# Optimization experiments

Hardware: AMD Instinct MI355X
Metric: run time of the kernel (lower is better)

The kernel has to match this reference:

```python
import jax, jax.numpy as jnp
import numpy as np
import math

B, S, D, H = 2, 2048, 1024, 16
DH = D // H          # 64 head dim
BLK = 64             # SpargeAttn block size
TOPK = 0.5           # fraction of KV blocks kept per query block
NEG = -1e9


def setup_inputs() -> dict:
    key = jax.random.key(0)
    ks = jax.random.split(key, 8)
    s = 0.02
    return {
        "inputs": jax.random.normal(ks[0], (B, S, D), dtype=jnp.float32),
        "ln_g": jnp.ones((D,), jnp.float32),
        "ln_b": jnp.zeros((D,), jnp.float32),
        "Wq": jax.random.normal(ks[1], (D, D), jnp.float32) * s,
        "bq": jnp.zeros((D,), jnp.float32),
        "Wk": jax.random.normal(ks[2], (D, D), jnp.float32) * s,
        "bk": jnp.zeros((D,), jnp.float32),
        "Wv": jax.random.normal(ks[3], (D, D), jnp.float32) * s,
        "bv": jnp.zeros((D,), jnp.float32),
        "Wo": jax.random.normal(ks[4], (D, D), jnp.float32) * s,
        "bo": jnp.zeros((D,), jnp.float32),
    }


def _sparse_topk_attn(q, k, v):
    # q,k,v: [B,H,S,DH]. Block-mean-similarity top-k sparse causal attention
    # (SpargeAttn spas_sage2_attn_meansim_topk, fp32 reference semantics).
    nb = S // BLK
    qm = q.reshape(B, H, nb, BLK, DH).mean(3)          # [B,H,nb,DH]
    km = k.reshape(B, H, nb, BLK, DH).mean(3)
    sim = jnp.einsum('bhqd,bhkd->bhqk', qm, km)        # block similarity
    cblk = jnp.tril(jnp.ones((nb, nb), bool))          # causal block mask
    sim = jnp.where(cblk, sim, NEG)
    kk = max(1, int(math.ceil(TOPK * nb)))
    _, idx = jax.lax.top_k(sim, kk)                    # [B,H,nb,kk]
    blk = jax.nn.one_hot(idx, nb, dtype=jnp.float32).sum(-2) > 0  # [B,H,nb,nb]
    blk = (blk & cblk) | jnp.eye(nb, dtype=bool)       # keep diagonal block
    tok_mask = jnp.repeat(jnp.repeat(blk, BLK, axis=2), BLK, axis=3)  # [B,H,S,S]
    tok_mask = tok_mask & jnp.tril(jnp.ones((S, S), bool))
    scores = jnp.einsum('bhid,bhjd->bhij', q, k) / jnp.float32(math.sqrt(DH))
    scores = jnp.where(tok_mask, scores, NEG)
    p = jax.nn.softmax(scores, axis=-1)
    return jnp.einsum('bhij,bhjd->bhid', p, v)


def reference(inputs, ln_g, ln_b, Wq, bq, Wk, bk, Wv, bv, Wo, bo):
    # pre-norm LayerNorm
    mu = inputs.mean(-1, keepdims=True)
    var = inputs.var(-1, keepdims=True)
    x = (inputs - mu) * jax.lax.rsqrt(var + 1e-5) * ln_g + ln_b
    # QKV projections -> [B,H,S,DH]
    q = (x @ Wq + bq).reshape(B, S, H, DH).transpose(0, 2, 1, 3)
    k = (x @ Wk + bk).reshape(B, S, H, DH).transpose(0, 2, 1, 3)
    v = (x @ Wv + bv).reshape(B, S, H, DH).transpose(0, 2, 1, 3)
    ctx = _sparse_topk_attn(q, k, v)
    ctx = ctx.transpose(0, 2, 1, 3).reshape(B, S, D)
    return ctx @ Wo + bo
```

## Files before the change

kernel.cpp:

```cpp
#include <hip/hip_runtime.h>
#include <stdint.h>

#define DEV static __device__ __forceinline__

typedef __attribute__((ext_vector_type(8))) short s16x8;
typedef __attribute__((ext_vector_type(4))) float f32x4;

constexpr int Bdim = 2, Sdim = 2048, Ddim = 1024, Hdim = 16, DH = 64;
constexpr int Mrows = Bdim * Sdim;
constexpr int NB = 32;
constexpr int SEL_STRIDE = 18;

constexpr size_t OFF_XB    = 0;
constexpr size_t OFF_WTQKV = OFF_XB    + (size_t)Mrows*Ddim*2;
constexpr size_t OFF_WOT   = OFF_WTQKV + (size_t)3072*1024*2;
constexpr size_t OFF_QKV   = OFF_WOT   + (size_t)1024*1024*2;
constexpr size_t OFF_CTX   = OFF_QKV   + (size_t)Mrows*3072*2;
constexpr size_t OFF_XM    = OFF_CTX   + (size_t)Mrows*Ddim*2;
constexpr size_t OFF_QM    = OFF_XM    + (size_t)64*1024*4;
constexpr size_t OFF_KM    = OFF_QM    + (size_t)64*1024*4;
constexpr size_t OFF_BIASQ = OFF_KM    + (size_t)64*1024*4;
constexpr size_t OFF_SEL   = OFF_BIASQ + (size_t)3072*4;
constexpr size_t OFF_PART  = OFF_SEL   + (size_t)1024*SEL_STRIDE*4;

DEV float bf2f(unsigned short u){ union{unsigned int i; float f;} x; x.i = ((unsigned int)u)<<16; return x.f; }
DEV unsigned short f2bf(float f){ union{float f; unsigned int i;} x; x.f=f;
  unsigned int r = x.i + 0x7fffu + ((x.i>>16)&1u); return (unsigned short)(r>>16); }

DEV void gload16(const unsigned short* g, unsigned short* l){
  __builtin_amdgcn_global_load_lds(
      (__attribute__((address_space(1))) void*)(void*)g,
      (__attribute__((address_space(3))) void*)l, 16, 0, 0);
}

DEV unsigned int cvtpk(float a, float b){
  unsigned int r;
  asm("v_cvt_pk_bf16_f32 %0, %1, %2" : "=v"(r) : "v"(a), "v"(b));
  return r;
}

__global__ __launch_bounds__(256) void ln_kernel(const float* __restrict__ inp,
                                                 const float* __restrict__ gam,
                                                 const float* __restrict__ bet,
                                                 unsigned short* __restrict__ xb){
  const int row = blockIdx.x, t = threadIdx.x;
  __shared__ float red[8];
  const float4 v = ((const float4*)(inp + (size_t)row*Ddim))[t];
  float s  = v.x + v.y + v.z + v.w;
  float s2 = v.x*v.x + v.y*v.y + v.z*v.z + v.w*v.w;
#pragma unroll
  for (int mk=32; mk>=1; mk>>=1){ s += __shfl_xor(s, mk); s2 += __shfl_xor(s2, mk); }
  if ((t&63)==0){ red[t>>6] = s; red[4+(t>>6)] = s2; }
  __syncthreads();
  s  = red[0]+red[1]+red[2]+red[3];
  s2 = red[4]+red[5]+red[6]+red[7];
  const float mu  = s * (1.f/Ddim);
  const float var = s2 * (1.f/Ddim) - mu*mu;
  const float rs  = rsqrtf(var + 1e-5f);
  const float4 gv = ((const float4*)gam)[t];
  const float4 bv = ((const float4*)bet)[t];
  float o0 = (v.x-mu)*rs*gv.x + bv.x;
  float o1 = (v.y-mu)*rs*gv.y + bv.y;
  float o2 = (v.z-mu)*rs*gv.z + bv.z;
  float o3 = (v.w-mu)*rs*gv.w + bv.w;
  uint2 u;
  u.x = (unsigned int)f2bf(o0) | ((unsigned int)f2bf(o1)<<16);
  u.y = (unsigned int)f2bf(o2) | ((unsigned int)f2bf(o3)<<16);
  ((uint2*)(xb + (size_t)row*Ddim))[t] = u;
}

__global__ __launch_bounds__(256) void xm_kernel(const float* __restrict__ inp,
                                                 const float* __restrict__ gam,
                                                 const float* __restrict__ bet,
                                                 float* __restrict__ xm){
  const int blk = blockIdx.x, t = threadIdx.x;
  const int w = t>>6, lane = t&63;
  __shared__ float part[4][1024];
  float4 gv[4], bv[4];
#pragma unroll
  for (int p=0;p<4;++p){ gv[p] = ((const float4*)gam)[lane + 64*p];
                         bv[p] = ((const float4*)bet)[lane + 64*p]; }
  float ax[4][4];
#pragma unroll
  for (int p=0;p<4;++p)
#pragma unroll
    for (int c=0;c<4;++c) ax[p][c]=0.f;
  for (int rr=0; rr<16; ++rr){
    const int row = blk*64 + w*16 + rr;
    const float4* rp = (const float4*)(inp + (size_t)row*Ddim);
    float4 v[4]; float s=0.f, s2=0.f;
#pragma unroll
    for (int p=0;p<4;++p){
      v[p] = rp[lane + 64*p];
      s  += v[p].x+v[p].y+v[p].z+v[p].w;
      s2 += v[p].x*v[p].x+v[p].y*v[p].y+v[p].z*v[p].z+v[p].w*v[p].w;
    }
#pragma unroll
    for (int mk=32; mk>=1; mk>>=1){ s += __shfl_xor(s,mk); s2 += __shfl_xor(s2,mk); }
    const float mu = s*(1.f/Ddim);
    const float var = s2*(1.f/Ddim) - mu*mu;
    const float rs = rsqrtf(var + 1e-5f);
#pragma unroll
    for (int p=0;p<4;++p){
      ax[p][0] += (v[p].x-mu)*rs*gv[p].x + bv[p].x;
      ax[p][1] += (v[p].y-mu)*rs*gv[p].y + bv[p].y;
      ax[p][2] += (v[p].z-mu)*rs*gv[p].z + bv[p].z;
      ax[p][3] += (v[p].w-mu)*rs*gv[p].w + bv[p].w;
    }
  }
#pragma unroll
  for (int p=0;p<4;++p){
    float4 o; o.x=ax[p][0]; o.y=ax[p][1]; o.z=ax[p][2]; o.w=ax[p][3];
    ((float4*)&part[w][0])[lane + 64*p] = o;
  }
  __syncthreads();
  float4 r0 = ((float4*)&part[0][0])[t];
  float4 r1 = ((float4*)&part[1][0])[t];
  float4 r2 = ((float4*)&part[2][0])[t];
  float4 r3 = ((float4*)&part[3][0])[t];
  float4 o;
  o.x = (r0.x+r1.x+r2.x+r3.x)*(1.f/64);
  o.y = (r0.y+r1.y+r2.y+r3.y)*(1.f/64);
  o.z = (r0.z+r1.z+r2.z+r3.z)*(1.f/64);
  o.w = (r0.w+r1.w+r2.w+r3.w)*(1.f/64);
  ((float4*)(xm + (size_t)blk*Ddim))[t] = o;
}

__global__ __launch_bounds__(256) void wtrans4_kernel(const float* __restrict__ Wq,
                                                      const float* __restrict__ Wk,
                                                      const float* __restrict__ Wv,
                                                      const float* __restrict__ Wo,
                                                      const float* __restrict__ bq,
                                                      const float* __restrict__ bk,
                                                      const float* __restrict__ bv,
                                                      unsigned short* __restrict__ wtqkv,
                                                      unsigned short* __restrict__ wot,
                                                      float* __restrict__ bqkv){
  __shared__ float tile[32][33];
  const int z = blockIdx.z;
  const float* W = (z==0)?Wq:(z==1)?Wk:(z==2)?Wv:Wo;
  unsigned short* Wt = (z<3) ? (wtqkv + (size_t)z*1024*1024) : wot;
  const int n0 = blockIdx.x*32, k0 = blockIdx.y*32;
  const int t = threadIdx.x, r = t>>5, c = t&31;
  if (z<3 && blockIdx.x==0 && blockIdx.y==0){
    const float* bb = (z==0)?bq:(z==1)?bk:bv;
#pragma unroll
    for (int i=0;i<4;++i) bqkv[z*1024 + t + 256*i] = bb[t + 256*i];
  }
#pragma unroll
  for (int i=0;i<4;++i) tile[r+8*i][c] = W[(size_t)(k0 + r + 8*i)*1024 + n0 + c];
  __syncthreads();
#pragma unroll
  for (int i=0;i<4;++i) Wt[(size_t)(n0 + r + 8*i)*1024 + k0 + c] = f2bf(tile[c][r+8*i]);
}

__global__ __launch_bounds__(256) void qmkm_part(const float* __restrict__ xm,
    const float* __restrict__ Wq, const float* __restrict__ Wk,
    float* __restrict__ part){
  const int c  = blockIdx.x*256 + threadIdx.x;
  const int rg = blockIdx.y >> 3, ks = blockIdx.y & 7;
  const int z  = blockIdx.z;
  const float* W = z ? Wk : Wq;
  const int r0 = rg*16, k0 = ks*128;
  float acc[16];
#pragma unroll
  for (int r=0;r<16;++r) acc[r]=0.f;
  for (int k=0;k<128;k+=4){
    const float wv0 = W[(size_t)(k0+k  )*1024 + c];
    const float wv1 = W[(size_t)(k0+k+1)*1024 + c];
    const float wv2 = W[(size_t)(k0+k+2)*1024 + c];
    const float wv3 = W[(size_t)(k0+k+3)*1024 + c];
#pragma unroll
    for (int r=0;r<16;++r){
      const float4 xv = *(const float4*)&xm[(size_t)(r0+r)*1024 + k0 + k];
      acc[r] = fmaf(xv.w, wv3, fmaf(xv.z, wv2, fmaf(xv.y, wv1, fmaf(xv.x, wv0, acc[r]))));
    }
  }
  float* dst = part + (((size_t)z*8 + ks)*64 + r0)*1024 + c;
#pragma unroll
  for (int r=0;r<16;++r) dst[(size_t)r*1024] = acc[r];
}

__global__ __launch_bounds__(256) void qmkm_reduce(const float* __restrict__ part,
    const float* __restrict__ bq, const float* __restrict__ bk,
    float* __restrict__ qm, float* __restrict__ km){
  const int idx = blockIdx.x*256 + threadIdx.x;
  const int z = blockIdx.y;
  const int c = idx & 1023, r = idx >> 10;
  const float* p = part + ((size_t)z*8*64*1024) + (size_t)r*1024 + c;
  float s = 0.f;
#pragma unroll
  for (int ks=0; ks<8; ++ks) s += p[(size_t)ks*64*1024];
  s += z ? bk[c] : bq[c];
  (z ? km : qm)[(size_t)r*1024 + c] = s;
}

__global__ __launch_bounds__(256) void topk_kernel(const float* __restrict__ qm,
                                                   const float* __restrict__ km,
                                                   int* __restrict__ sel){
  const int bhq = blockIdx.x;
  const int qb = bhq & 31, h = (bhq>>5) & 15, b = bhq >> 9;
  const int t = threadIdx.x;
  __shared__ float sim[32];
  __shared__ int keep[32];
  const int kb = t>>3, l8 = t&7;
  float acc = 0.f;
  if (kb <= qb){
    const float* qv = qm + (size_t)(b*32 + qb)*1024 + h*64;
    const float* kv = km + (size_t)(b*32 + kb)*1024 + h*64;
#pragma unroll
    for (int d=0; d<8; ++d) acc += qv[l8*8+d] * kv[l8*8+d];
  }
  acc += __shfl_xor(acc,1); acc += __shfl_xor(acc,2); acc += __shfl_xor(acc,4);
  if (l8==0) sim[kb] = (kb<=qb) ? acc : -1e30f;
  __syncthreads();
  if (t < 32){
    int k2 = t; int ok = 0;
    if (k2 <= qb){
      float sv = sim[k2]; int rank = 0;
      for (int j=0;j<=qb;++j){
        float sj = sim[j];
        rank += (sj > sv) || (sj == sv && j < k2);
      }
      ok = (rank < 16) || (k2 == qb);
    }
    keep[t] = ok;
  }
  __syncthreads();
  if (t == 0){
    int* dstp = sel + (size_t)bhq * SEL_STRIDE;
    int c = 0;
    for (int j=0;j<32;++j) if (keep[j]) dstp[1+c++] = j;
    dstp[0] = c;
  }
}

#define G_STAGE(bsel, kofs) do { \
  gload16(A0 + (kofs), ldsA + (bsel)*4096 + (wid*2+0)*512); \
  gload16(A1 + (kofs), ldsA + (bsel)*4096 + (wid*2+1)*512); \
  gload16(B0 + (kofs), ldsB + (bsel)*4096 + (wid*2+0)*512); \
  gload16(B1 + (kofs), ldsB + (bsel)*4096 + (wid*2+1)*512); \
} while(0)

#define G_COMPUTE(bsel) do { \
  s16x8 af[4], bfr[4]; \
  _Pragma("unroll") \
  for (int mi=0;mi<4;++mi){ \
    int row = wr*64 + mi*16 + rl; \
    af[mi] = *(const s16x8*)((char*)ldsA + (bsel)*8192 + row*64 + ((g ^ ((row>>1)&3))<<4)); \
  } \
  _Pragma("unroll") \
  for (int ni=0;ni<4;++ni){ \
    int row = wc*64 + ni*16 + rl; \
    bfr[ni] = *(const s16x8*)((char*)ldsB + (bsel)*8192 + row*64 + ((g ^ ((row>>1)&3))<<4)); \
  } \
  _Pragma("unroll") \
  for (int mi=0;mi<4;++mi) \
    _Pragma("unroll") \
    for (int ni=0;ni<4;++ni) \
      acc[mi][ni] = __builtin_amdgcn_mfma_f32_16x16x32_bf16(af[mi], bfr[ni], acc[mi][ni], 0,0,0); \
} while(0)

template<int OUT_BF16>
__global__ __launch_bounds__(256) void gemm_bt(const unsigned short* __restrict__ A,
                                               const unsigned short* __restrict__ Bt,
                                               const float* __restrict__ bias,
                                               void* __restrict__ C, int N){
  constexpr int K = 1024;
  __shared__ unsigned short ldsA[2*128*32];
  __shared__ unsigned short ldsB[2*128*32];
  const int t = threadIdx.x, lane = t & 63, wid = t >> 6;
  const int wr = wid >> 1, wc = wid & 1;
  const int rl = lane & 15, g = lane >> 4;

  const int nbx = gridDim.x;
  const int nwg = nbx * gridDim.y;
  const int id  = blockIdx.y * nbx + blockIdx.x;
  const int nid = (id & 7) * (nwg >> 3) + (id >> 3);
  const int m0 = (nid / nbx) * 128, n0 = (nid % nbx) * 128;

  const f32x4 ZERO4 = {0.f,0.f,0.f,0.f};
  f32x4 acc[4][4];
#pragma unroll
  for (int i=0;i<4;++i)
#pragma unroll
    for (int j=0;j<4;++j) acc[i][j] = ZERO4;

  const int slot0 = wid*128 + lane, slot1 = slot0 + 64;
  const int sr0 = slot0>>2, sc0 = slot0&3;
  const int sr1 = slot1>>2, sc1 = slot1&3;
  const unsigned short* A0 = A  + (size_t)(m0 + sr0)*K + (sc0 ^ ((sr0>>1)&3))*8;
  const unsigned short* A1 = A  + (size_t)(m0 + sr1)*K + (sc1 ^ ((sr1>>1)&3))*8;
  const unsigned short* B0 = Bt + (size_t)(n0 + sr0)*K + (sc0 ^ ((sr0>>1)&3))*8;
  const unsigned short* B1 = Bt + (size_t)(n0 + sr1)*K + (sc1 ^ ((sr1>>1)&3))*8;

  G_STAGE(0, 0);
  __syncthreads();

  for (int k0=0; k0<K; k0+=64){
    G_STAGE(1, k0+32);
    G_COMPUTE(0);
    __syncthreads();
    if (k0+64 < K) G_STAGE(0, k0+64);
    G_COMPUTE(1);
    __syncthreads();
  }

  const int r4 = g*4;
#pragma unroll
  for (int mi=0;mi<4;++mi){
#pragma unroll
    for (int ni=0;ni<4;++ni){
      int col = n0 + wc*64 + ni*16 + rl;
      float bb = bias[col];
#pragma unroll
      for (int e=0;e<4;++e){
        int row = m0 + wr*64 + mi*16 + r4 + e;
        float v = acc[mi][ni][e] + bb;
        if (OUT_BF16) ((unsigned short*)C)[(size_t)row*N + col] = f2bf(v);
        else          ((float*)C)[(size_t)row*N + col] = v;
      }
    }
  }
}

__global__ __launch_bounds__(256) void attn_kernel(const unsigned short* __restrict__ qkv,
                                                   const int* __restrict__ sel,
                                                   unsigned short* __restrict__ ctx){
  const int id = blockIdx.x;
  const int xcd = id & 7, jj = id >> 3;
  const int bh = xcd + 8*(jj/24);
  const int tau = jj % 24;
  const int h = bh & 15, b = bh >> 4;
  int qbl[2]; int nq;
  if (tau < 8){ qbl[0]=tau; qbl[1]=15-tau; nq=2; }
  else        { qbl[0]=tau+8; qbl[1]=0;    nq=1; }

  const int t = threadIdx.x, wid = t >> 6, lane = t & 63;
  const int rl = lane & 15, g = lane >> 4;
  const int q_local = wid*16 + rl;

  __shared__ unsigned short K_s[2][4096];
  __shared__ unsigned short V_s[2][4096];

  const int jst = t >> 2, cq = t & 3;
  const int r2 = t >> 3, dq = t & 7;
  const unsigned short* kbase = qkv + (size_t)(b*Sdim + jst)*3072 + 1024 + h*DH + cq*16;
  const unsigned short* vbase = qkv + (size_t)(b*Sdim + 2*r2)*3072 + 2048 + h*DH + dq*8;
  const int kwb0 = jst*128 + (((cq*2  ) ^ (jst&7))<<4);
  const int kwb1 = jst*128 + (((cq*2+1) ^ (jst&7))<<4);
  const f32x4 ZERO4 = {0.f,0.f,0.f,0.f};

  const int src0 = (rl + 16*((2*g  ) & 3)) << 2;
  const int src1 = (rl + 16*((2*g+1) & 3)) << 2;
  const bool hsel = (g >> 1);

  for (int iq=0; iq<nq; ++iq){
    const int qb = qbl[iq];
    const int* selrow = sel + (size_t)(((b*Hdim)+h)*NB + qb) * SEL_STRIDE;
    const int ns = selrow[0];

    const int qg0 = b*Sdim + qb*64 + q_local;
    const unsigned short* qbase = qkv + (size_t)qg0*3072 + h*DH;
    s16x8 qa[2];
#pragma unroll
    for (int kk=0; kk<2; ++kk){
      s16x8 raw = *(const s16x8*)(qbase + kk*32 + g*8);
      s16x8 qq;
#pragma unroll
      for (int e=0;e<8;++e) qq[e] = (short)f2bf(bf2f((unsigned short)raw[e]) * 0.125f);
      qa[kk] = qq;
    }

    f32x4 o[4];
    float m_r = -3.0e38f, l_r = 0.f;
#pragma unroll
    for (int f=0; f<4; ++f) o[f] = ZERO4;

    __syncthreads();

    int kb = selrow[1];
    s16x8 kr0, kr1, vr0, vr1;
    {
      const size_t off = (size_t)kb*64*3072;
      kr0 = *(const s16x8*)(kbase + off);
      kr1 = *(const s16x8*)(kbase + off + 8);
      vr0 = *(const s16x8*)(vbase + off);
      vr1 = *(const s16x8*)(vbase + off + 3072);
    }

    for (int it=0; it<ns; ++it){
      const int buf = it & 1;
      unsigned short* Kw = &K_s[buf][0];
      unsigned short* Vw = &V_s[buf][0];
      *(s16x8*)((char*)Kw + kwb0) = kr0;
      *(s16x8*)((char*)Kw + kwb1) = kr1;
#pragma unroll
      for (int e=0;e<8;++e){
        const int d1 = dq*8 + e;
        const int sw = (d1&7) ^ (d1>>3);
        const unsigned int pr = (unsigned int)(unsigned short)vr0[e]
                              | ((unsigned int)(unsigned short)vr1[e] << 16);
        *(unsigned int*)((char*)Vw + d1*128 + ((4*r2) ^ (sw<<4))) = pr;
      }
      const int kbcur = kb;
      if (it+1 < ns){
        kb = selrow[2+it];
        const size_t off = (size_t)kb*64*3072;
        kr0 = *(const s16x8*)(kbase + off);
        kr1 = *(const s16x8*)(kbase + off + 8);
        vr0 = *(const s16x8*)(vbase + off);
        vr1 = *(const s16x8*)(vbase + off + 3072);
      }
      __syncthreads();

      f32x4 sfT[4];
#pragma unroll
      for (int f=0;f<4;++f) sfT[f] = ZERO4;
#pragma unroll
      for (int kk=0;kk<2;++kk){
#pragma unroll
        for (int f=0;f<4;++f){
          const int jr = f*16 + rl;
          s16x8 kf = *(const s16x8*)((char*)Kw + jr*128 + (((kk*4+g) ^ (jr&7))<<4));
          sfT[f] = __builtin_amdgcn_mfma_f32_16x16x32_bf16(kf, qa[kk], sfT[f], 0,0,0);
        }
      }
      if (kbcur == qb){
#pragma unroll
        for (int f=0;f<4;++f)
#pragma unroll
          for (int e=0;e<4;++e){
            const int j = f*16 + g*4 + e;
            if (j > q_local) sfT[f][e] = -1e9f;
          }
      }
      {
        float mx = sfT[0][0];
#pragma unroll
        for (int f=0;f<4;++f)
#pragma unroll
          for (int e=0;e<4;++e) mx = fmaxf(mx, sfT[f][e]);
        mx = fmaxf(mx, __shfl_xor(mx, 16));
        mx = fmaxf(mx, __shfl_xor(mx, 32));
        const float mn = fmaxf(m_r, mx);
        const float al = __expf(m_r - mn);
        m_r = mn;
        float rs = 0.f;
#pragma unroll
        for (int f=0;f<4;++f)
#pragma unroll
          for (int e=0;e<4;++e){
            const float p = __expf(sfT[f][e] - mn);
            sfT[f][e] = p; rs += p;
          }
        rs += __shfl_xor(rs, 16);
        rs += __shfl_xor(rs, 32);
        l_r = l_r*al + rs;
#pragma unroll
        for (int f=0;f<4;++f)
#pragma unroll
          for (int e=0;e<4;++e) o[f][e] *= al;
      }

      unsigned int plo[4], phi[4];
#pragma unroll
      for (int f=0;f<4;++f){
        plo[f] = cvtpk(sfT[f][0], sfT[f][1]);
        phi[f] = cvtpk(sfT[f][2], sfT[f][3]);
      }

#pragma unroll
      for (int kk=0;kk<2;++kk){
        const int f0 = 2*kk, f1 = 2*kk+1;
        unsigned int a0, b0, w0, w1, w2, w3;
        a0 = __builtin_amdgcn_ds_bpermute(src0, plo[f0]);
        b0 = __builtin_amdgcn_ds_bpermute(src0, plo[f1]);
        w0 = hsel ? b0 : a0;
        a0 = __builtin_amdgcn_ds_bpermute(src0, phi[f0]);
        b0 = __builtin_amdgcn_ds_bpermute(src0, phi[f1]);
        w1 = hsel ? b0 : a0;
        a0 = __builtin_amdgcn_ds_bpermute(src1, plo[f0]);
        b0 = __builtin_amdgcn_ds_bpermute(src1, plo[f1]);
        w2 = hsel ? b0 : a0;
        a0 = __builtin_amdgcn_ds_bpermute(src1, phi[f0]);
        b0 = __builtin_amdgcn_ds_bpermute(src1, phi[f1]);
        w3 = hsel ? b0 : a0;
        union { unsigned int u[4]; s16x8 v; } pfc;
        pfc.u[0] = w0; pfc.u[1] = w1; pfc.u[2] = w2; pfc.u[3] = w3;
        const s16x8 pf = pfc.v;
#pragma unroll
        for (int f=0;f<4;++f){
          const int d = f*16 + rl;
          const int sw = (d&7) ^ (d>>3);
          s16x8 vf = *(const s16x8*)((char*)Vw + d*128 + ((64*kk + 16*g) ^ (sw<<4)));
          o[f] = __builtin_amdgcn_mfma_f32_16x16x32_bf16(vf, pf, o[f], 0,0,0);
        }
      }
    }

    {
      const float inv = 1.f / l_r;
      unsigned short* crow = ctx + (size_t)qg0*Ddim + h*DH;
#pragma unroll
      for (int f=0;f<4;++f){
        uint2 st;
        st.x = (unsigned int)f2bf(o[f][0]*inv) | ((unsigned int)f2bf(o[f][1]*inv)<<16);
        st.y = (unsigned int)f2bf(o[f][2]*inv) | ((unsigned int)f2bf(o[f][3]*inv)<<16);
        *(uint2*)(crow + f*16 + g*4) = st;
      }
    }
  }
}

extern "C" void kernel_launch(void* const* d_in, const int* in_sizes, int n_in,
                              void* d_out, int out_size, void* d_ws, size_t ws_size,
                              hipStream_t stream){
  (void)in_sizes; (void)n_in; (void)out_size; (void)ws_size;
  const float* inp  = (const float*)d_in[0];
  const float* ln_g = (const float*)d_in[1];
  const float* ln_b = (const float*)d_in[2];
  const float* Wq   = (const float*)d_in[3];
  const float* bq   = (const float*)d_in[4];
  const float* Wk   = (const float*)d_in[5];
  const float* bk   = (const float*)d_in[6];
  const float* Wv   = (const float*)d_in[7];
  const float* bv   = (const float*)d_in[8];
  const float* Wo   = (const float*)d_in[9];
  const float* bo   = (const float*)d_in[10];

  char* ws = (char*)d_ws;
  unsigned short* xb    = (unsigned short*)(ws + OFF_XB);
  unsigned short* wtqkv = (unsigned short*)(ws + OFF_WTQKV);
  unsigned short* wot   = (unsigned short*)(ws + OFF_WOT);
  unsigned short* qkvb  = (unsigned short*)(ws + OFF_QKV);
  unsigned short* ctx   = (unsigned short*)(ws + OFF_CTX);
  float* xm   = (float*)(ws + OFF_XM);
  float* qm   = (float*)(ws + OFF_QM);
  float* km   = (float*)(ws + OFF_KM);
  float* bqkv = (float*)(ws + OFF_BIASQ);
  int*   sel  = (int*)(ws + OFF_SEL);
  float* part = (float*)(ws + OFF_PART);

  ln_kernel<<<Mrows, 256, 0, stream>>>(inp, ln_g, ln_b, xb);
  xm_kernel<<<64, 256, 0, stream>>>(inp, ln_g, ln_b, xm);
  wtrans4_kernel<<<dim3(32,32,4), 256, 0, stream>>>(Wq, Wk, Wv, Wo, bq, bk, bv, wtqkv, wot, bqkv);
  qmkm_part<<<dim3(4,32,2), 256, 0, stream>>>(xm, Wq, Wk, part);
  qmkm_reduce<<<dim3(256,2), 256, 0, stream>>>(part, bq, bk, qm, km);
  topk_kernel<<<1024, 256, 0, stream>>>(qm, km, sel);
  gemm_bt<1><<<dim3(24,32), 256, 0, stream>>>(xb, wtqkv, bqkv, (void*)qkvb, 3072);
  attn_kernel<<<768, 256, 0, stream>>>(qkvb, sel, ctx);
  gemm_bt<0><<<dim3(8,32), 256, 0, stream>>>(ctx, wot, bo, d_out, 1024);
}
```

Baseline: 164.0 us.

## Pipeline GEMM K-loop with explicit vmcnt waits, remap tiles per XCD, add MFMA priority

```diff
diff --git a/kernel.cpp b/kernel.cpp
--- a/kernel.cpp
+++ b/kernel.cpp
@@ -267,24 +267,27 @@
                                                const float* __restrict__ bias,
                                                void* __restrict__ C, int N){
   constexpr int K = 1024;
+  constexpr int NT = K/32;
   __shared__ unsigned short ldsA[2*128*32];
   __shared__ unsigned short ldsB[2*128*32];
   const int t = threadIdx.x, lane = t & 63, wid = t >> 6;
   const int wr = wid >> 1, wc = wid & 1;
   const int rl = lane & 15, g = lane >> 4;
 
-  const int nbx = gridDim.x;
-  const int nwg = nbx * gridDim.y;
+  const int nbx = gridDim.x, nby = gridDim.y;
   const int id  = blockIdx.y * nbx + blockIdx.x;
-  const int nid = (id & 7) * (nwg >> 3) + (id >> 3);
-  const int m0 = (nid / nbx) * 128, n0 = (nid % nbx) * 128;
+  const int xcd = id & 7, j = id >> 3;
+  const int MBP = nby >> 2, NBP = nbx >> 1;
+  const int mg = xcd >> 1, ng = xcd & 1;
+  const int m0 = (mg*MBP + (j % MBP)) * 128;
+  const int n0 = (ng*NBP + (j / MBP)) * 128;
 
   const f32x4 ZERO4 = {0.f,0.f,0.f,0.f};
   f32x4 acc[4][4];
 #pragma unroll
   for (int i=0;i<4;++i)
 #pragma unroll
-    for (int j=0;j<4;++j) acc[i][j] = ZERO4;
+    for (int j2=0;j2<4;++j2) acc[i][j2] = ZERO4;
 
   const int slot0 = wid*128 + lane, slot1 = slot0 + 64;
   const int sr0 = slot0>>2, sc0 = slot0&3;
@@ -295,15 +298,20 @@
   const unsigned short* B1 = Bt + (size_t)(n0 + sr1)*K + (sc1 ^ ((sr1>>1)&3))*8;
 
   G_STAGE(0, 0);
-  __syncthreads();
-
-  for (int k0=0; k0<K; k0+=64){
-    G_STAGE(1, k0+32);
-    G_COMPUTE(0);
-    __syncthreads();
-    if (k0+64 < K) G_STAGE(0, k0+64);
-    G_COMPUTE(1);
-    __syncthreads();
+
+  for (int ti=0; ti<NT; ++ti){
+    const int cur = ti & 1;
+    if (ti+1 < NT){
+      G_STAGE(cur^1, (ti+1)*32);
+      asm volatile("s_waitcnt vmcnt(4)" ::: "memory");
+    } else {
+      asm volatile("s_waitcnt vmcnt(0)" ::: "memory");
+    }
+    __builtin_amdgcn_s_barrier();
+    __builtin_amdgcn_sched_barrier(0);
+    G_COMPUTE(cur);
+    __builtin_amdgcn_sched_barrier(0);
+    __builtin_amdgcn_s_barrier();
   }
 
   const int r4 = g*4;
@@ -417,6 +425,7 @@
       f32x4 sfT[4];
 #pragma unroll
       for (int f=0;f<4;++f) sfT[f] = ZERO4;
+      __builtin_amdgcn_s_setprio(1);
 #pragma unroll
       for (int kk=0;kk<2;++kk){
 #pragma unroll
@@ -426,13 +435,14 @@
           sfT[f] = __builtin_amdgcn_mfma_f32_16x16x32_bf16(kf, qa[kk], sfT[f], 0,0,0);
         }
       }
+      __builtin_amdgcn_s_setprio(0);
       if (kbcur == qb){
 #pragma unroll
         for (int f=0;f<4;++f)
 #pragma unroll
           for (int e=0;e<4;++e){
-            const int j = f*16 + g*4 + e;
-            if (j > q_local) sfT[f][e] = -1e9f;
+            const int j2 = f*16 + g*4 + e;
+            if (j2 > q_local) sfT[f][e] = -1e9f;
           }
       }
       {
@@ -489,6 +499,7 @@
         union { unsigned int u[4]; s16x8 v; } pfc;
         pfc.u[0] = w0; pfc.u[1] = w1; pfc.u[2] = w2; pfc.u[3] = w3;
         const s16x8 pf = pfc.v;
+        __builtin_amdgcn_s_setprio(1);
 #pragma unroll
         for (int f=0;f<4;++f){
           const int d = f*16 + rl;
@@ -496,6 +507,7 @@
           s16x8 vf = *(const s16x8*)((char*)Vw + d*128 + ((64*kk + 16*g) ^ (sw<<4)));
           o[f] = __builtin_amdgcn_mfma_f32_16x16x32_bf16(vf, pf, o[f], 0,0,0);
         }
+        __builtin_amdgcn_s_setprio(0);
       }
     }
 
```

After: 146.7 us. 10.5% less time.
